# Kernel tuning notes

Measured on AMD Instinct MI355X. Metric: run time of the kernel, lower is better.

Reference implementation:

```python
import jax, jax.numpy as jnp
import numpy as np

B, S, D, H = 2, 2048, 1024, 16  # batch, seq, embed_dim, num_heads
DH = D // H                      # head dim = 64


def setup_inputs() -> dict:
    key = jax.random.key(0)
    kx, kq, kbq, kk, kbk, kv, kbv = jax.random.split(key, 7)
    scale = 1.0 / np.sqrt(D)
    return {
        "x": jax.random.normal(kx, (B, S, D), dtype=jnp.float32),
        "Wq": jax.random.normal(kq, (D, D), dtype=jnp.float32) * scale,
        "bq": jax.random.normal(kbq, (D,), dtype=jnp.float32) * 0.01,
        "Wk": jax.random.normal(kk, (D, D), dtype=jnp.float32) * scale,
        "bk": jax.random.normal(kbk, (D,), dtype=jnp.float32) * 0.01,
        "Wv": jax.random.normal(kv, (D, D), dtype=jnp.float32) * scale,
        "bv": jax.random.normal(kbv, (D,), dtype=jnp.float32) * 0.01,
    }


def reference(x, Wq, bq, Wk, bk, Wv, bv):
    # ooqkv_type == 'q', odeint_method == 'id': q branch = act(Linear(x)), exact GELU (torch nn.GELU default)
    q = jax.nn.gelu(x @ Wq + bq, approximate=False)
    k = x @ Wk + bk
    v = x @ Wv + bv
    # [B, S, D] -> [B, S, H, DH]
    q = q.reshape(B, S, H, DH)
    k = k.reshape(B, S, H, DH)
    v = v.reshape(B, S, H, DH)
    # NOTE: original module has NO 1/sqrt(d) scale — faithful reproduction
    att = jnp.einsum("bqhd,bkhd->bhqk", q, k)
    att = jax.nn.softmax(att, axis=-1)
    out = jnp.einsum("bhqk,bkhd->bqhd", att, v)
    return out.reshape(B, S, D)
```

## Files before the change

### kernel.cpp

```cpp
#include <hip/hip_runtime.h>
#include <math.h>

#define B_  2
#define S_  2048
#define D_  1024
#define H_  16
#define DH_ 64
#define M_  (B_ * S_)

typedef _Float16 half_t;
typedef __attribute__((ext_vector_type(8))) _Float16 h8;
typedef __attribute__((ext_vector_type(4))) _Float16 h4;
typedef __attribute__((ext_vector_type(4))) float   f32x4;

#define LOG2E 1.44269504088896f

__device__ __forceinline__ void gll16(const half_t* g, half_t* l) {
    __builtin_amdgcn_global_load_lds(
        (__attribute__((address_space(1))) const void*)g,
        (__attribute__((address_space(3))) void*)l, 16, 0, 0);
}

__global__ __launch_bounds__(256) void prep_k(
    const float* __restrict__ x, half_t* __restrict__ xh,
    const float* __restrict__ Wq, const float* __restrict__ Wk,
    const float* __restrict__ Wv, half_t* __restrict__ Wt)
{
    const int bx = blockIdx.x;
    if (bx < 2048) {
        const size_t i = ((size_t)bx * 256 + threadIdx.x) * 8;
        const float4 a = *(const float4*)(x + i);
        const float4 b = *(const float4*)(x + i + 4);
        h8 o;
        o[0] = (half_t)a.x; o[1] = (half_t)a.y; o[2] = (half_t)a.z; o[3] = (half_t)a.w;
        o[4] = (half_t)b.x; o[5] = (half_t)b.y; o[6] = (half_t)b.z; o[7] = (half_t)b.w;
        *(h8*)(xh + i) = o;
    } else {
        const int gb    = bx - 2048;
        const int which = gb >> 9;
        const float* __restrict__ W = (which == 0) ? Wq : (which == 1) ? Wk : Wv;
        half_t* __restrict__ T = Wt + (size_t)which * D_ * D_;
        const int gw   = (gb & 511) * 4 + (threadIdx.x >> 6);
        const int lane = threadIdx.x & 63;
        const int n    = (gw & 15) * 64 + lane;
        const int k0   = (gw >> 4) * 8;
        h8 o;
        #pragma unroll
        for (int t = 0; t < 8; ++t) o[t] = (half_t)W[(size_t)(k0 + t) * D_ + n];
        *(h8*)(T + (size_t)n * D_ + k0) = o;
    }
}

__global__ __launch_bounds__(256) void qkv_gemm_f16(
    const half_t* __restrict__ xh, const half_t* __restrict__ Wt,
    const float* __restrict__ bq, const float* __restrict__ bk,
    const float* __restrict__ bv,
    half_t* __restrict__ Qo, half_t* __restrict__ Ko, half_t* __restrict__ Vt)
{
    const int lin = blockIdx.y * 24 + blockIdx.x;
    const int swz = (lin & 7) * 96 + (lin >> 3);
    const int n0g = (swz % 24) * 128;
    const int m0  = (swz / 24) * 128;
    const int which = n0g >> 10;
    const int n0    = n0g & 1023;
    const half_t* __restrict__ Wp  = Wt + (size_t)which * D_ * D_;
    const float* __restrict__ bias = (which == 0) ? bq : (which == 1) ? bk : bv;

    const int tid = threadIdx.x, lane = tid & 63, wave = tid >> 6;
    const int wm = (wave >> 1) * 64, wn = (wave & 1) * 64;
    const int ln = lane & 15, quad = lane >> 4;

    __shared__ __align__(16) half_t SMEM[128 * 136];
    half_t* const As = SMEM;
    half_t* const Bs = SMEM + 128 * 64;

    const int r0  = tid >> 3, c0 = tid & 7;
    const int cs  = c0 ^ (r0 & 7);
    const half_t* aS = xh + (size_t)(m0 + r0) * D_ + cs * 8;
    const half_t* bS = Wp + (size_t)(n0 + r0) * D_ + cs * 8;

    f32x4 acc[4][4];
    #pragma unroll
    for (int i = 0; i < 4; ++i)
        #pragma unroll
        for (int j = 0; j < 4; ++j) acc[i][j] = (f32x4){0.f, 0.f, 0.f, 0.f};

    for (int k0 = 0; k0 < D_; k0 += 64) {
        __syncthreads();
        #pragma unroll
        for (int l = 0; l < 4; ++l) {
            gll16(aS + (size_t)l * 32 * D_, &As[(tid + l * 256) * 8]);
            gll16(bS + (size_t)l * 32 * D_, &Bs[(tid + l * 256) * 8]);
        }
        aS += 64; bS += 64;
        __syncthreads();

        #pragma unroll
        for (int kc = 0; kc < 2; ++kc) {
            h8 af[4], bf[4];
            #pragma unroll
            for (int i = 0; i < 4; ++i) {
                const int r = wm + i * 16 + ln;
                af[i] = *(const h8*)&As[r * 64 + (((kc << 2) + quad) ^ (r & 7)) * 8];
            }
            #pragma unroll
            for (int j = 0; j < 4; ++j) {
                const int r = wn + j * 16 + ln;
                bf[j] = *(const h8*)&Bs[r * 64 + (((kc << 2) + quad) ^ (r & 7)) * 8];
            }
            #pragma unroll
            for (int i = 0; i < 4; ++i)
                #pragma unroll
                for (int j = 0; j < 4; ++j)
                    acc[i][j] = __builtin_amdgcn_mfma_f32_16x16x32_f16(
                        af[i], bf[j], acc[i][j], 0, 0, 0);
        }
    }

    if (which == 2) {
        #pragma unroll
        for (int j = 0; j < 4; ++j) {
            const int col = n0 + wn + j * 16 + ln;
            const int h = col >> 6, d = col & 63;
            const float bb = bias[col];
            #pragma unroll
            for (int i = 0; i < 4; ++i) {
                const int sg = m0 + wm + i * 16 + quad * 4;
                const int b  = sg >> 11, srow = sg & 2047;
                h4 pv;
                #pragma unroll
                for (int r = 0; r < 4; ++r) pv[r] = (half_t)(acc[i][j][r] + bb);
                *(h4*)(Vt + (((size_t)(b * H_ + h) * DH_ + d) * S_ + srow)) = pv;
            }
        }
    } else {
        half_t* __restrict__ outp = (which == 0) ? Qo : Ko;
        __syncthreads();
        #pragma unroll
        for (int j = 0; j < 4; ++j) {
            const int col = wn + j * 16 + ln;
            const float bb = bias[n0 + col];
            #pragma unroll
            for (int i = 0; i < 4; ++i) {
                #pragma unroll
                for (int r = 0; r < 4; ++r) {
                    const int row = wm + i * 16 + quad * 4 + r;
                    float t = acc[i][j][r] + bb;
                    if (which == 0) {
                        const float u = t * fmaf(t * t, 0.0356774081f, 0.7978845608f);
                        const float e = __builtin_amdgcn_exp2f(u * -2.88539008178f);
                        t = t * __builtin_amdgcn_rcpf(1.0f + e) * LOG2E;
                    }
                    SMEM[row * 136 + col] = (half_t)t;
                }
            }
        }
        __syncthreads();
        const int cc = tid & 15;
        const int rr = tid >> 4;
        #pragma unroll
        for (int p = 0; p < 8; ++p) {
            const int row = p * 16 + rr;
            const h8 v = *(const h8*)&SMEM[row * 136 + cc * 8];
            *(h8*)(outp + (size_t)(m0 + row) * D_ + n0 + cc * 8) = v;
        }
    }
}

#define ATTN_TILE(KS, VS)                                                     \
    do {                                                                      \
        f32x4 sa[4];                                                          \
        __builtin_amdgcn_s_setprio(1);                                        \
        _Pragma("unroll")                                                     \
        for (int j = 0; j < 4; ++j) {                                         \
            const int rK = j * 16 + ln;                                       \
            const h8 ka0 = *(const h8*)&KS[rK * 64 + ((quad)     ^ (rK & 7)) * 8]; \
            const h8 ka1 = *(const h8*)&KS[rK * 64 + ((quad + 4) ^ (rK & 7)) * 8]; \
            f32x4 t = (f32x4){0.f, 0.f, 0.f, 0.f};                            \
            t = __builtin_amdgcn_mfma_f32_16x16x32_f16(ka0, qa0, t, 0, 0, 0); \
            t = __builtin_amdgcn_mfma_f32_16x16x32_f16(ka1, qa1, t, 0, 0, 0); \
            sa[j] = t;                                                        \
        }                                                                     \
        __builtin_amdgcn_s_setprio(0);                                        \
        float mxa = sa[0][0];                                                 \
        _Pragma("unroll")                                                     \
        for (int j = 0; j < 4; ++j)                                           \
            _Pragma("unroll")                                                 \
            for (int r = 0; r < 4; ++r) mxa = fmaxf(mxa, sa[j][r]);           \
        mxa = fmaxf(mxa, __shfl_xor(mxa, 16, 64));                            \
        mxa = fmaxf(mxa, __shfl_xor(mxa, 32, 64));                            \
        if (__ballot(mxa > m_a)) {                                            \
            const float mna = fmaxf(m_a, mxa);                                \
            const float ala = __builtin_amdgcn_exp2f(m_a - mna);              \
            m_a = mna;                                                        \
            float ra[4];                                                      \
            _Pragma("unroll")                                                 \
            for (int r = 0; r < 4; ++r) ra[r] = __shfl(ala, quad * 4 + r, 64);\
            _Pragma("unroll")                                                 \
            for (int r = 0; r < 4; ++r) {                                     \
                la[r] *= ra[r];                                               \
                _Pragma("unroll")                                             \
                for (int j = 0; j < 4; ++j) Oa[j][r] *= ra[r];                \
            }                                                                 \
        }                                                                     \
        _Pragma("unroll")                                                     \
        for (int j = 0; j < 4; ++j) {                                         \
            h4 pva;                                                           \
            _Pragma("unroll")                                                 \
            for (int r = 0; r < 4; ++r)                                       \
                pva[r] = (half_t)__builtin_amdgcn_exp2f(sa[j][r] - m_a);      \
            *(h4*)&QPs[wave * 16 + ln][j * 16 + quad * 4] = pva;              \
        }                                                                     \
        const h8 pa0 = *(const h8*)&QPs[wave * 16 + ln][quad * 8];            \
        const h8 pa1 = *(const h8*)&QPs[wave * 16 + ln][32 + quad * 8];       \
        __builtin_amdgcn_s_setprio(1);                                        \
        _Pragma("unroll")                                                     \
        for (int j = 0; j < 4; ++j) {                                         \
            const int rV = j * 16 + ln;                                       \
            const h8 vb0 = *(const h8*)&VS[rV * 64 + ((quad)     ^ (rV & 7)) * 8]; \
            const h8 vb1 = *(const h8*)&VS[rV * 64 + ((quad + 4) ^ (rV & 7)) * 8]; \
            Oa[j] = __builtin_amdgcn_mfma_f32_16x16x32_f16(pa0, vb0, Oa[j], 0, 0, 0); \
            Oa[j] = __builtin_amdgcn_mfma_f32_16x16x32_f16(pa1, vb1, Oa[j], 0, 0, 0); \
        }                                                                     \
        la = __builtin_amdgcn_mfma_f32_16x16x32_f16(pa0, ones8, la, 0, 0, 0); \
        la = __builtin_amdgcn_mfma_f32_16x16x32_f16(pa1, ones8, la, 0, 0, 0); \
        __builtin_amdgcn_s_setprio(0);                                        \
    } while (0)

__global__ __launch_bounds__(512) void attn_f16(
    const half_t* __restrict__ Q, const half_t* __restrict__ K,
    const half_t* __restrict__ Vt, float* __restrict__ out)
{
    const int tid  = threadIdx.x;
    const int lane = tid & 63;
    const int wave = tid >> 6;
    const int ln   = lane & 15;
    const int quad = lane >> 4;

    const int lin = blockIdx.y * 16 + blockIdx.x;
    const int swz = (lin & 7) * 64 + (lin >> 3);
    const int bh  = swz >> 4;
    const int b   = bh >> 4;
    const int h   = bh & 15;
    const int q0  = (swz & 15) * 128;

    const half_t* __restrict__ Qb  = Q  + (size_t)b * S_ * D_ + h * DH_;
    const half_t* __restrict__ Kb  = K  + (size_t)b * S_ * D_ + h * DH_;
    const half_t* __restrict__ Vtb = Vt + (size_t)bh * DH_ * S_;

    __shared__ __align__(16) half_t Ks0[64 * 64];
    __shared__ __align__(16) half_t Vs0[64 * 64];
    __shared__ __align__(16) half_t Ks1[64 * 64];
    __shared__ __align__(16) half_t Vs1[64 * 64];
    __shared__ __align__(16) half_t QPs[128][72];

    const int sr  = tid >> 3, sc0 = tid & 7;
    const int scs = sc0 ^ (sr & 7);
    const half_t* kS = Kb  + (size_t)sr * D_ + scs * 8;
    const half_t* vS = Vtb + (size_t)sr * S_ + scs * 8;
    half_t* const kD0 = &Ks0[tid * 8];
    half_t* const vD0 = &Vs0[tid * 8];
    half_t* const kD1 = &Ks1[tid * 8];
    half_t* const vD1 = &Vs1[tid * 8];

    gll16(kS, kD0); gll16(vS, vD0);
    kS += 64 * D_; vS += 64;

    #pragma unroll
    for (int l = 0; l < 2; ++l) {
        const int c = tid + l * 512;
        const int r = c >> 3, k8 = c & 7;
        *(h8*)&QPs[r][k8 * 8] = *(const h8*)(Qb + (size_t)(q0 + r) * D_ + k8 * 8);
    }
    __syncthreads();
    const h8 qa0 = *(const h8*)&QPs[wave * 16 + ln][quad * 8];
    const h8 qa1 = *(const h8*)&QPs[wave * 16 + ln][32 + quad * 8];

    h8 ones8;
    #pragma unroll
    for (int t = 0; t < 8; ++t) ones8[t] = (half_t)1.0f;

    f32x4 Oa[4];
    #pragma unroll
    for (int j = 0; j < 4; ++j) Oa[j] = (f32x4){0.f, 0.f, 0.f, 0.f};
    f32x4 la = (f32x4){0.f, 0.f, 0.f, 0.f};
    float m_a = -INFINITY;

    for (int it = 0; it < 16; ++it) {
        gll16(kS, kD1); gll16(vS, vD1);
        kS += 64 * D_; vS += 64;
        ATTN_TILE(Ks0, Vs0);
        __syncthreads();

        if (it < 15) {
            gll16(kS, kD0); gll16(vS, vD0);
            kS += 64 * D_; vS += 64;
        }
        ATTN_TILE(Ks1, Vs1);
        __syncthreads();
    }

    #pragma unroll
    for (int r = 0; r < 4; ++r) {
        const float iva = 1.0f / la[r];
        const int rowa = q0 + wave * 16 + quad * 4 + r;
        #pragma unroll
        for (int j = 0; j < 4; ++j)
            out[((size_t)b * S_ + rowa) * D_ + h * DH_ + j * 16 + ln] = Oa[j][r] * iva;
    }
}

extern "C" void kernel_launch(void* const* d_in, const int* in_sizes, int n_in,
                              void* d_out, int out_size, void* d_ws, size_t ws_size,
                              hipStream_t stream) {
    const float* x  = (const float*)d_in[0];
    const float* Wq = (const float*)d_in[1];
    const float* bq = (const float*)d_in[2];
    const float* Wk = (const float*)d_in[3];
    const float* bk = (const float*)d_in[4];
    const float* Wv = (const float*)d_in[5];
    const float* bv = (const float*)d_in[6];
    float* out = (float*)d_out;

    const size_t nmd = (size_t)M_ * D_;
    const size_t ndd = (size_t)D_ * D_;
    half_t* xh  = (half_t*)d_ws;
    half_t* Wt  = xh + nmd;
    half_t* Qh  = Wt + 3 * ndd;
    half_t* Kh  = Qh + nmd;
    half_t* Vtw = Kh + nmd;

    prep_k<<<2048 + 1536, 256, 0, stream>>>(x, xh, Wq, Wk, Wv, Wt);
    qkv_gemm_f16<<<dim3(3 * D_ / 128, M_ / 128), 256, 0, stream>>>(
        xh, Wt, bq, bk, bv, Qh, Kh, Vtw);
    attn_f16<<<dim3(S_ / 128, B_ * H_), 512, 0, stream>>>(Qh, Kh, Vtw, out);
}
```

Measured before the change: 178.0 us.

## Fuse x fp32-to-fp16 conversion into QKV GEMM and defer softmax rescaling

Drops the separate x conversion pass in the prep kernel. The QKV GEMM now loads fp32 x directly, converts it in registers and writes fp16 into LDS, while W still uses global_load_lds. This removes a round trip of x through global memory, but x is now read at twice the bytes per tile, and the A-tile load becomes synchronous register staging, so it overlaps less with the async load. Separately, the attention online softmax only rescales when the running max grows by more than a threshold, skipping most rescale work. That risks fp16 P overflow or loss of precision when the max grows by up to the threshold without being rescaled.

```diff
diff --git a/kernel.cpp b/kernel.cpp
--- a/kernel.cpp
+++ b/kernel.cpp
@@ -22,37 +22,25 @@
 }
 
 __global__ __launch_bounds__(256) void prep_k(
-    const float* __restrict__ x, half_t* __restrict__ xh,
     const float* __restrict__ Wq, const float* __restrict__ Wk,
     const float* __restrict__ Wv, half_t* __restrict__ Wt)
 {
-    const int bx = blockIdx.x;
-    if (bx < 2048) {
-        const size_t i = ((size_t)bx * 256 + threadIdx.x) * 8;
-        const float4 a = *(const float4*)(x + i);
-        const float4 b = *(const float4*)(x + i + 4);
-        h8 o;
-        o[0] = (half_t)a.x; o[1] = (half_t)a.y; o[2] = (half_t)a.z; o[3] = (half_t)a.w;
-        o[4] = (half_t)b.x; o[5] = (half_t)b.y; o[6] = (half_t)b.z; o[7] = (half_t)b.w;
-        *(h8*)(xh + i) = o;
-    } else {
-        const int gb    = bx - 2048;
-        const int which = gb >> 9;
-        const float* __restrict__ W = (which == 0) ? Wq : (which == 1) ? Wk : Wv;
-        half_t* __restrict__ T = Wt + (size_t)which * D_ * D_;
-        const int gw   = (gb & 511) * 4 + (threadIdx.x >> 6);
-        const int lane = threadIdx.x & 63;
-        const int n    = (gw & 15) * 64 + lane;
-        const int k0   = (gw >> 4) * 8;
-        h8 o;
-        #pragma unroll
-        for (int t = 0; t < 8; ++t) o[t] = (half_t)W[(size_t)(k0 + t) * D_ + n];
-        *(h8*)(T + (size_t)n * D_ + k0) = o;
-    }
+    const int gb    = blockIdx.x;
+    const int which = gb >> 9;
+    const float* __restrict__ W = (which == 0) ? Wq : (which == 1) ? Wk : Wv;
+    half_t* __restrict__ T = Wt + (size_t)which * D_ * D_;
+    const int gw   = (gb & 511) * 4 + (threadIdx.x >> 6);
+    const int lane = threadIdx.x & 63;
+    const int n    = (gw & 15) * 64 + lane;
+    const int k0   = (gw >> 4) * 8;
+    h8 o;
+    #pragma unroll
+    for (int t = 0; t < 8; ++t) o[t] = (half_t)W[(size_t)(k0 + t) * D_ + n];
+    *(h8*)(T + (size_t)n * D_ + k0) = o;
 }
 
 __global__ __launch_bounds__(256) void qkv_gemm_f16(
-    const half_t* __restrict__ xh, const half_t* __restrict__ Wt,
+    const float* __restrict__ x, const half_t* __restrict__ Wt,
     const float* __restrict__ bq, const float* __restrict__ bk,
     const float* __restrict__ bv,
     half_t* __restrict__ Qo, half_t* __restrict__ Ko, half_t* __restrict__ Vt)
@@ -76,7 +64,7 @@
 
     const int r0  = tid >> 3, c0 = tid & 7;
     const int cs  = c0 ^ (r0 & 7);
-    const half_t* aS = xh + (size_t)(m0 + r0) * D_ + cs * 8;
+    const float*  aS = x  + (size_t)(m0 + r0) * D_ + cs * 8;
     const half_t* bS = Wp + (size_t)(n0 + r0) * D_ + cs * 8;
 
     f32x4 acc[4][4];
@@ -87,10 +75,23 @@
 
     for (int k0 = 0; k0 < D_; k0 += 64) {
         __syncthreads();
+        float4 av[4][2];
         #pragma unroll
         for (int l = 0; l < 4; ++l) {
-            gll16(aS + (size_t)l * 32 * D_, &As[(tid + l * 256) * 8]);
+            av[l][0] = *(const float4*)(aS + (size_t)l * 32 * D_);
+            av[l][1] = *(const float4*)(aS + (size_t)l * 32 * D_ + 4);
+        }
+        #pragma unroll
+        for (int l = 0; l < 4; ++l)
             gll16(bS + (size_t)l * 32 * D_, &Bs[(tid + l * 256) * 8]);
+        #pragma unroll
+        for (int l = 0; l < 4; ++l) {
+            h8 o;
+            o[0] = (half_t)av[l][0].x; o[1] = (half_t)av[l][0].y;
+            o[2] = (half_t)av[l][0].z; o[3] = (half_t)av[l][0].w;
+            o[4] = (half_t)av[l][1].x; o[5] = (half_t)av[l][1].y;
+            o[6] = (half_t)av[l][1].z; o[7] = (half_t)av[l][1].w;
+            *(h8*)&As[(tid + l * 256) * 8] = o;
         }
         aS += 64; bS += 64;
         __syncthreads();
@@ -167,6 +168,7 @@
     }
 }
 
+#define DEFER_THR 10.0f
 #define ATTN_TILE(KS, VS)                                                     \
     do {                                                                      \
         f32x4 sa[4];                                                          \
@@ -189,7 +191,7 @@
             for (int r = 0; r < 4; ++r) mxa = fmaxf(mxa, sa[j][r]);           \
         mxa = fmaxf(mxa, __shfl_xor(mxa, 16, 64));                            \
         mxa = fmaxf(mxa, __shfl_xor(mxa, 32, 64));                            \
-        if (__ballot(mxa > m_a)) {                                            \
+        if (__ballot(mxa > m_a + DEFER_THR)) {                                \
             const float mna = fmaxf(m_a, mxa);                                \
             const float ala = __builtin_amdgcn_exp2f(m_a - mna);              \
             m_a = mna;                                                        \
@@ -324,14 +326,13 @@
 
     const size_t nmd = (size_t)M_ * D_;
     const size_t ndd = (size_t)D_ * D_;
-    half_t* xh  = (half_t*)d_ws;
-    half_t* Wt  = xh + nmd;
+    half_t* Wt  = (half_t*)d_ws;
     half_t* Qh  = Wt + 3 * ndd;
     half_t* Kh  = Qh + nmd;
     half_t* Vtw = Kh + nmd;
 
-    prep_k<<<2048 + 1536, 256, 0, stream>>>(x, xh, Wq, Wk, Wv, Wt);
+    prep_k<<<1536, 256, 0, stream>>>(Wq, Wk, Wv, Wt);
     qkv_gemm_f16<<<dim3(3 * D_ / 128, M_ / 128), 256, 0, stream>>>(
-        xh, Wt, bq, bk, bv, Qh, Kh, Vtw);
+        x, Wt, bq, bk, bv, Qh, Kh, Vtw);
     attn_f16<<<dim3(S_ / 128, B_ * H_), 512, 0, stream>>>(Qh, Kh, Vtw, out);
 }
```

Measured after the change: 190.0 us. 6.7% more time.
